# Performance work log

Measured on AMD Instinct MI355X. Metric: run time of the kernel, lower is better.

Reference implementation:

```python
import jax, jax.numpy as jnp
import numpy as np
import math

S, B, D = 2048, 2, 1024
H = 16
DH = D // H
WIN = 256
DIL = 1


def setup_inputs() -> dict:
    key = jax.random.key(0)
    ks = jax.random.split(key, 10)
    std = 1.0 / math.sqrt(D)
    return {
        "x": jax.random.normal(ks[0], (S, B, D), jnp.float32),
        "beta": jax.random.normal(ks[1], (H,), jnp.float32) * 0.02,
        "Wq": jax.random.normal(ks[2], (D, D), jnp.float32) * std,
        "bq": jnp.zeros((D,), jnp.float32),
        "Wk": jax.random.normal(ks[3], (D, D), jnp.float32) * std,
        "bk": jnp.zeros((D,), jnp.float32),
        "Wv": jax.random.normal(ks[4], (D, D), jnp.float32) * std,
        "bv": jnp.zeros((D,), jnp.float32),
        "Wo": jax.random.normal(ks[5], (D, D), jnp.float32) * std,
        "bo": jnp.zeros((D,), jnp.float32),
    }


def _split_heads(t):
    # (S, B, D) -> (B*H, S, DH), matching rearrange 's b (h d) -> (b h) s d'
    return t.reshape(S, B, H, DH).transpose(1, 2, 0, 3).reshape(B * H, S, DH)


def reference(x, beta, Wq, bq, Wk, bk, Wv, bv, Wo, bo):
    q = _split_heads(x @ Wq + bq)
    k = _split_heads(x @ Wk + bk)
    v = _split_heads(x @ Wv + bv)

    # per-head learnable temperature: q / (sqrt(d_head) * exp(beta))
    beta_exp = jnp.tile(jnp.exp(beta), B)  # (B*H,), head index = z % H
    q = q / (jnp.sqrt(jnp.asarray(DH, x.dtype)) * beta_exp)[:, None, None]

    # causal dilated windowed mask
    idx = jnp.arange(S)
    diff = idx[:, None] - idx[None, :]
    allowed = (diff >= 0) & (diff <= DIL * (WIN - 1)) & (diff % DIL == 0)
    mask = jnp.where(allowed, jnp.asarray(0.0, x.dtype), jnp.asarray(-jnp.inf, x.dtype))

    scores = jnp.einsum('zqd,zkd->zqk', q, k) + mask[None]
    # attention sink: extra zero-logit column absorbing probability mass
    scores = jnp.concatenate([scores, jnp.zeros((B * H, S, 1), scores.dtype)], axis=-1)
    attn = jax.nn.softmax(scores, axis=-1)[..., :-1]

    out = jnp.einsum('zqk,zkd->zqd', attn, v)
    # (B*H, S, DH) -> (S, B, D)
    out = out.reshape(B, H, S, DH).transpose(2, 0, 1, 3).reshape(S, B, D)
    return out @ Wo + bo
```

## Files before the change

kernel.cpp:

```cpp
#include <hip/hip_runtime.h>
#include <math.h>

#define S_LEN  2048
#define BATCH  2
#define DM     1024
#define NHEAD  16
#define DHEAD  64
#define WIN    256
#define MROWS  4096

#define KP   72
#define PPAD 68

typedef __attribute__((ext_vector_type(8))) short bf16x8;
typedef __attribute__((ext_vector_type(4))) float f32x4;

__device__ __forceinline__ unsigned short f2b(float f) {
    unsigned int u = __float_as_uint(f);
    return (unsigned short)((u + 0x7fffu + ((u >> 16) & 1u)) >> 16);
}
__device__ __forceinline__ void gld16(const void* g, void* l) {
    __builtin_amdgcn_global_load_lds(
        (const __attribute__((address_space(1))) void*)g,
        (__attribute__((address_space(3))) void*)l, 16, 0, 0);
}
__device__ __forceinline__ bf16x8 pack8(float4 a, float4 b) {
    bf16x8 r;
    r[0] = (short)f2b(a.x); r[1] = (short)f2b(a.y);
    r[2] = (short)f2b(a.z); r[3] = (short)f2b(a.w);
    r[4] = (short)f2b(b.x); r[5] = (short)f2b(b.y);
    r[6] = (short)f2b(b.z); r[7] = (short)f2b(b.w);
    return r;
}

__global__ __launch_bounds__(256)
void cvtx(const float* __restrict__ x, unsigned short* __restrict__ xb)
{
    const int i = (blockIdx.x * 256 + threadIdx.x) * 4;
    float4 f = *(const float4*)(x + i);
    ushort4 o; o.x = f2b(f.x); o.y = f2b(f.y); o.z = f2b(f.z); o.w = f2b(f.w);
    *(ushort4*)(xb + i) = o;
}

__global__ __launch_bounds__(256)
void twcvt4(const float* __restrict__ W0, const float* __restrict__ W1,
            const float* __restrict__ W2, const float* __restrict__ W3,
            unsigned short* __restrict__ T0, unsigned short* __restrict__ T1,
            unsigned short* __restrict__ T2, unsigned short* __restrict__ T3)
{
    const int zz = blockIdx.z;
    const float* W = (zz == 0) ? W0 : (zz == 1) ? W1 : (zz == 2) ? W2 : W3;
    unsigned short* WT = (zz == 0) ? T0 : (zz == 1) ? T1 : (zz == 2) ? T2 : T3;

    __shared__ float t32[32][33];
    const int bx = blockIdx.x * 32;
    const int by = blockIdx.y * 32;
    const int c  = threadIdx.x & 31;
    const int r0 = threadIdx.x >> 5;
#pragma unroll
    for (int p = 0; p < 4; ++p)
        t32[r0 + 8 * p][c] = W[(size_t)(by + r0 + 8 * p) * DM + bx + c];
    __syncthreads();
#pragma unroll
    for (int p = 0; p < 4; ++p)
        WT[(size_t)(bx + r0 + 8 * p) * DM + by + c] = f2b(t32[c][r0 + 8 * p]);
}

__global__ __launch_bounds__(256)
void gemm_mfma(const unsigned short* __restrict__ A,
               const unsigned short* __restrict__ BT,
               const float* __restrict__ bias,
               const float* __restrict__ bias2,
               const float* __restrict__ beta,
               float* __restrict__ Cf,
               unsigned short* __restrict__ Cb,
               int mode)
{
    __shared__ unsigned short As[128 * 32];
    __shared__ unsigned short Bs[128 * 32];

    const int t  = threadIdx.x;
    const int wv = t >> 6, ln = t & 63;
    const int rowBase = blockIdx.y * 128;
    const int colBase = blockIdx.x * 128;

    const int m16 = ln & 15, g = ln >> 4;
    const int wr = wv >> 1, wc = wv & 1;
    const int swz = m16 & 3;

    const int lr = ln >> 2;
    const int lq = (ln & 3) ^ (lr & 3);
    const unsigned short* ga = A  + (size_t)(rowBase + wv * 16 + lr) * DM + lq * 8;
    const unsigned short* gb = BT + (size_t)(colBase + wv * 16 + lr) * DM + lq * 8;
    unsigned short* la0 = As + wv * 512;
    unsigned short* la1 = la0 + 2048;
    unsigned short* lb0 = Bs + wv * 512;
    unsigned short* lb1 = lb0 + 2048;

    f32x4 acc[4][4];
#pragma unroll
    for (int u = 0; u < 4; ++u)
#pragma unroll
        for (int v = 0; v < 4; ++v)
            acc[u][v] = (f32x4){0.f, 0.f, 0.f, 0.f};

    for (int kb = 0; kb < DM; kb += 32) {
        gld16(ga + kb, la0);
        gld16(ga + (size_t)64 * DM + kb, la1);
        gld16(gb + kb, lb0);
        gld16(gb + (size_t)64 * DM + kb, lb1);
        __syncthreads();

        bf16x8 af[4], bfr[4];
#pragma unroll
        for (int u = 0; u < 4; ++u)
            af[u] = *(const bf16x8*)&As[(wr * 64 + u * 16 + m16) * 32 + ((g ^ swz) * 8)];
#pragma unroll
        for (int v = 0; v < 4; ++v)
            bfr[v] = *(const bf16x8*)&Bs[(wc * 64 + v * 16 + m16) * 32 + ((g ^ swz) * 8)];
#pragma unroll
        for (int u = 0; u < 4; ++u)
#pragma unroll
            for (int v = 0; v < 4; ++v)
                acc[u][v] = __builtin_amdgcn_mfma_f32_16x16x32_bf16(
                    af[u], bfr[v], acc[u][v], 0, 0, 0);
        __syncthreads();
    }

    const int q4 = g * 4;
    if (mode == 0) {
#pragma unroll
        for (int v = 0; v < 4; ++v) {
            const int col = colBase + wc * 64 + v * 16 + m16;
            const float bi = bias[col];
#pragma unroll
            for (int u = 0; u < 4; ++u)
#pragma unroll
                for (int r = 0; r < 4; ++r) {
                    const int row = rowBase + wr * 64 + u * 16 + q4 + r;
                    Cf[(size_t)row * DM + col] = acc[u][v][r] + bi;
                }
        }
    } else if (mode == 1) {
#pragma unroll
        for (int v = 0; v < 4; ++v) {
            const int col  = colBase + wc * 64 + v * 16 + m16;
            const bool isq = (col < DM);
            const int h    = (col >> 6) & (NHEAD - 1);
            const int dh   = col & 63;
            const float bi = isq ? bias[col] : bias2[col - DM];
            const float sc = isq ? 0.125f * __expf(-beta[h]) : 1.0f;
            unsigned short* base = Cb + (isq ? 0 : (size_t)MROWS * DM);
#pragma unroll
            for (int u = 0; u < 4; ++u)
#pragma unroll
                for (int r = 0; r < 4; ++r) {
                    const int row = rowBase + wr * 64 + u * 16 + q4 + r;
                    const int s = row >> 1, bb = row & 1;
                    const int z = bb * NHEAD + h;
                    base[((size_t)z * S_LEN + s) * DHEAD + dh] =
                        f2b((acc[u][v][r] + bi) * sc);
                }
        }
    } else {
#pragma unroll
        for (int u = 0; u < 4; ++u)
#pragma unroll
            for (int r = 0; r < 4; ++r) {
                const int row = rowBase + wr * 64 + u * 16 + q4 + r;
                const int hh = row >> 6, dh = row & 63;
                const float bi = bias[row];
#pragma unroll
                for (int v = 0; v < 4; ++v) {
                    const int col = colBase + wc * 64 + v * 16 + m16;
                    const int s = col >> 1, bb = col & 1;
                    Cb[((size_t)(bb * NHEAD + hh) * DHEAD + dh) * S_LEN + s] =
                        f2b(acc[u][v][r] + bi);
                }
            }
    }
}

__global__ __launch_bounds__(256, 4)
void attn_mfma(const unsigned short* __restrict__ q,
               const unsigned short* __restrict__ k,
               const unsigned short* __restrict__ vt,
               unsigned short* __restrict__ ao)
{
    __shared__ unsigned short Ks[64 * KP];
    __shared__ unsigned short Vs[64 * KP];
    __shared__ float Ps[64][PPAD];

    const int t   = threadIdx.x;
    const int wv  = t >> 6, ln = t & 63;
    const int m16 = ln & 15, g = ln >> 4;
    const int z   = blockIdx.y;
    const int q0  = blockIdx.x * 64;
    const size_t zbase = (size_t)z * S_LEN * DHEAD;

    const unsigned short* qrow = q + zbase + (size_t)(q0 + wv * 16 + m16) * DHEAD;
    bf16x8 qf0 = *(const bf16x8*)(qrow + g * 8);
    bf16x8 qf1 = *(const bf16x8*)(qrow + 32 + g * 8);

    f32x4 oacc[4];
#pragma unroll
    for (int v4 = 0; v4 < 4; ++v4) oacc[v4] = (f32x4){0.f, 0.f, 0.f, 0.f};
    float mr[4], lr[4];
#pragma unroll
    for (int r = 0; r < 4; ++r) { mr[r] = 0.f; lr[r] = 1.f; }

    for (int c = 0; c < 5; ++c) {
        const int kb = q0 - 256 + c * 64;
        if (kb < 0) continue;
        __syncthreads();

#pragma unroll
        for (int i = 0; i < 2; ++i) {
            const int id  = t + 256 * i;
            const int row = id >> 3;
            const int co  = (id & 7) * 8;
            *(bf16x8*)&Ks[row * KP + co] =
                *(const bf16x8*)(k + zbase + (size_t)(kb + row) * DHEAD + co);
            *(bf16x8*)&Vs[row * KP + co] =
                *(const bf16x8*)(vt + ((size_t)z * DHEAD + row) * S_LEN + kb + co);
        }
        __syncthreads();

        f32x4 sacc[4];
#pragma unroll
        for (int v4 = 0; v4 < 4; ++v4) {
            sacc[v4] = (f32x4){0.f, 0.f, 0.f, 0.f};
            bf16x8 kf0 = *(const bf16x8*)&Ks[(v4 * 16 + m16) * KP + g * 8];
            sacc[v4] = __builtin_amdgcn_mfma_f32_16x16x32_bf16(qf0, kf0, sacc[v4], 0, 0, 0);
            bf16x8 kf1 = *(const bf16x8*)&Ks[(v4 * 16 + m16) * KP + 32 + g * 8];
            sacc[v4] = __builtin_amdgcn_mfma_f32_16x16x32_bf16(qf1, kf1, sacc[v4], 0, 0, 0);
        }

        const bool mhi = (c == 4), mlo = (c == 0);
#pragma unroll
        for (int r = 0; r < 4; ++r) {
            const int ig = q0 + wv * 16 + g * 4 + r;
            float sv[4];
            float smax = -1e30f;
#pragma unroll
            for (int v4 = 0; v4 < 4; ++v4) {
                const int jg = kb + v4 * 16 + m16;
                float x = sacc[v4][r];
                const bool valid = (!mhi || jg <= ig) && (!mlo || jg >= ig - (WIN - 1));
                x = valid ? x : -1e30f;
                sv[v4] = x;
                smax = fmaxf(smax, x);
            }
#pragma unroll
            for (int off = 1; off < 16; off <<= 1)
                smax = fmaxf(smax, __shfl_xor(smax, off, 64));
            const float mnew  = fmaxf(mr[r], smax);
            const float alpha = __expf(mr[r] - mnew);
            float rsum = 0.f;
#pragma unroll
            for (int v4 = 0; v4 < 4; ++v4) {
                const float pp = __expf(sv[v4] - mnew);
                Ps[wv * 16 + g * 4 + r][v4 * 16 + m16] = pp;
                rsum += pp;
            }
#pragma unroll
            for (int off = 1; off < 16; off <<= 1)
                rsum += __shfl_xor(rsum, off, 64);
            lr[r] = lr[r] * alpha + rsum;
            mr[r] = mnew;
#pragma unroll
            for (int v4 = 0; v4 < 4; ++v4) oacc[v4][r] *= alpha;
        }
        __syncthreads();

        const float* prow = &Ps[wv * 16 + m16][0];
        bf16x8 pf0 = pack8(*(const float4*)(prow + g * 8),
                           *(const float4*)(prow + g * 8 + 4));
        bf16x8 pf1 = pack8(*(const float4*)(prow + 32 + g * 8),
                           *(const float4*)(prow + 32 + g * 8 + 4));
#pragma unroll
        for (int v4 = 0; v4 < 4; ++v4) {
            bf16x8 vf0 = *(const bf16x8*)&Vs[(v4 * 16 + m16) * KP + g * 8];
            oacc[v4] = __builtin_amdgcn_mfma_f32_16x16x32_bf16(pf0, vf0, oacc[v4], 0, 0, 0);
            bf16x8 vf1 = *(const bf16x8*)&Vs[(v4 * 16 + m16) * KP + 32 + g * 8];
            oacc[v4] = __builtin_amdgcn_mfma_f32_16x16x32_bf16(pf1, vf1, oacc[v4], 0, 0, 0);
        }
    }

    const int bb = z >> 4, h = z & 15;
#pragma unroll
    for (int r = 0; r < 4; ++r) {
        const int ig  = q0 + wv * 16 + g * 4 + r;
        const float inv = 1.f / lr[r];
#pragma unroll
        for (int v4 = 0; v4 < 4; ++v4)
            ao[(size_t)(ig * BATCH + bb) * DM + h * DHEAD + v4 * 16 + m16] =
                f2b(oacc[v4][r] * inv);
    }
}

extern "C" void kernel_launch(void* const* d_in, const int* in_sizes, int n_in,
                              void* d_out, int out_size, void* d_ws, size_t ws_size,
                              hipStream_t stream)
{
    const float* x    = (const float*)d_in[0];
    const float* beta = (const float*)d_in[1];
    const float* Wq   = (const float*)d_in[2];
    const float* bq   = (const float*)d_in[3];
    const float* Wk   = (const float*)d_in[4];
    const float* bk   = (const float*)d_in[5];
    const float* Wv   = (const float*)d_in[6];
    const float* bv   = (const float*)d_in[7];
    const float* Wo   = (const float*)d_in[8];
    const float* bo   = (const float*)d_in[9];
    float* out = (float*)d_out;

    unsigned short* w = (unsigned short*)d_ws;
    const size_t seg = (size_t)MROWS * DM;
    unsigned short* qb  = w;
    unsigned short* kbf = w + seg;
    unsigned short* vtb = w + 2 * seg;
    unsigned short* ab  = w + 3 * seg;
    unsigned short* xb  = w + 4 * seg;
    unsigned short* wtq = w + 5 * seg;
    unsigned short* wtk = wtq + (size_t)DM * DM;
    unsigned short* wtv = wtk + (size_t)DM * DM;
    unsigned short* wto = wtv + (size_t)DM * DM;

    cvtx<<<4096, 256, 0, stream>>>(x, xb);
    twcvt4<<<dim3(32, 32, 4), 256, 0, stream>>>(Wq, Wk, Wv, Wo, wtq, wtk, wtv, wto);

    gemm_mfma<<<dim3(2048 / 128, MROWS / 128), 256, 0, stream>>>(
        xb, wtq, bq, bk, beta, nullptr, qb, 1);
    gemm_mfma<<<dim3(MROWS / 128, DM / 128), 256, 0, stream>>>(
        wtv, xb, bv, nullptr, beta, nullptr, vtb, 3);

    attn_mfma<<<dim3(S_LEN / 64, BATCH * NHEAD), 256, 0, stream>>>(qb, kbf, vtb, ab);

    gemm_mfma<<<dim3(DM / 128, MROWS / 128), 256, 0, stream>>>(
        ab, wto, bo, nullptr, beta, out, nullptr, 0);
}
```

Baseline: 194.3 us.

## Fuse V projection into QKV GEMM and transpose V in a separate kernel

The V projection moves into the same GEMM launch as Q and K, widened to 3072 output columns, so all three write head-split bf16 rows. This replaces the separate V GEMM, whose transposed epilogue wrote scattered strided values. A small LDS-based vtrans kernel then transposes V into the (z, dh, s) layout attention expects, with coalesced 16-byte stores. It reuses the x bf16 buffer for V^T and adds one kernel launch plus an extra round trip of V through memory.

```diff
diff --git a/kernel.cpp b/kernel.cpp
--- a/kernel.cpp
+++ b/kernel.cpp
@@ -67,10 +67,38 @@
 }
 
 __global__ __launch_bounds__(256)
+void vtrans(const unsigned short* __restrict__ v, unsigned short* __restrict__ vt)
+{
+    __shared__ unsigned short T[64 * 72];
+    const int z  = blockIdx.y;
+    const int s0 = blockIdx.x * 64;
+    const int t  = threadIdx.x;
+#pragma unroll
+    for (int i = 0; i < 2; ++i) {
+        const int id = t + 256 * i;
+        const int r  = id >> 3;
+        const int c8 = (id & 7) * 8;
+        *(bf16x8*)&T[r * 72 + c8] =
+            *(const bf16x8*)(v + ((size_t)z * S_LEN + s0 + r) * DHEAD + c8);
+    }
+    __syncthreads();
+    const int dh = t & 63, sg = t >> 6;
+#pragma unroll
+    for (int i = 0; i < 2; ++i) {
+        const int sb = (sg + 4 * i) * 8;
+        bf16x8 o;
+#pragma unroll
+        for (int e = 0; e < 8; ++e) o[e] = T[(sb + e) * 72 + dh];
+        *(bf16x8*)(vt + ((size_t)z * DHEAD + dh) * S_LEN + s0 + sb) = o;
+    }
+}
+
+__global__ __launch_bounds__(256)
 void gemm_mfma(const unsigned short* __restrict__ A,
                const unsigned short* __restrict__ BT,
-               const float* __restrict__ bias,
-               const float* __restrict__ bias2,
+               const float* __restrict__ b0,
+               const float* __restrict__ b1,
+               const float* __restrict__ b2,
                const float* __restrict__ beta,
                float* __restrict__ Cf,
                unsigned short* __restrict__ Cb,
@@ -132,7 +160,7 @@
 #pragma unroll
         for (int v = 0; v < 4; ++v) {
             const int col = colBase + wc * 64 + v * 16 + m16;
-            const float bi = bias[col];
+            const float bi = b0[col];
 #pragma unroll
             for (int u = 0; u < 4; ++u)
 #pragma unroll
@@ -141,16 +169,16 @@
                     Cf[(size_t)row * DM + col] = acc[u][v][r] + bi;
                 }
         }
-    } else if (mode == 1) {
+    } else {
 #pragma unroll
         for (int v = 0; v < 4; ++v) {
-            const int col  = colBase + wc * 64 + v * 16 + m16;
-            const bool isq = (col < DM);
-            const int h    = (col >> 6) & (NHEAD - 1);
-            const int dh   = col & 63;
-            const float bi = isq ? bias[col] : bias2[col - DM];
-            const float sc = isq ? 0.125f * __expf(-beta[h]) : 1.0f;
-            unsigned short* base = Cb + (isq ? 0 : (size_t)MROWS * DM);
+            const int col = colBase + wc * 64 + v * 16 + m16;
+            const int sec = col >> 10;
+            const int h   = (col >> 6) & (NHEAD - 1);
+            const int dh  = col & 63;
+            const float bi = (sec == 0 ? b0 : sec == 1 ? b1 : b2)[col & (DM - 1)];
+            const float sc = (sec == 0) ? 0.125f * __expf(-beta[h]) : 1.0f;
+            unsigned short* base = Cb + (size_t)sec * MROWS * DM;
 #pragma unroll
             for (int u = 0; u < 4; ++u)
 #pragma unroll
@@ -162,22 +190,6 @@
                         f2b((acc[u][v][r] + bi) * sc);
                 }
         }
-    } else {
-#pragma unroll
-        for (int u = 0; u < 4; ++u)
-#pragma unroll
-            for (int r = 0; r < 4; ++r) {
-                const int row = rowBase + wr * 64 + u * 16 + q4 + r;
-                const int hh = row >> 6, dh = row & 63;
-                const float bi = bias[row];
-#pragma unroll
-                for (int v = 0; v < 4; ++v) {
-                    const int col = colBase + wc * 64 + v * 16 + m16;
-                    const int s = col >> 1, bb = col & 1;
-                    Cb[((size_t)(bb * NHEAD + hh) * DHEAD + dh) * S_LEN + s] =
-                        f2b(acc[u][v][r] + bi);
-                }
-            }
     }
 }
 
@@ -318,25 +330,26 @@
     unsigned short* w = (unsigned short*)d_ws;
     const size_t seg = (size_t)MROWS * DM;
     unsigned short* qb  = w;
-    unsigned short* kbf = w + seg;
-    unsigned short* vtb = w + 2 * seg;
+    unsigned short* kb  = w + seg;
+    unsigned short* vb  = w + 2 * seg;
     unsigned short* ab  = w + 3 * seg;
     unsigned short* xb  = w + 4 * seg;
     unsigned short* wtq = w + 5 * seg;
     unsigned short* wtk = wtq + (size_t)DM * DM;
     unsigned short* wtv = wtk + (size_t)DM * DM;
     unsigned short* wto = wtv + (size_t)DM * DM;
+    unsigned short* vtb = xb;
 
     cvtx<<<4096, 256, 0, stream>>>(x, xb);
     twcvt4<<<dim3(32, 32, 4), 256, 0, stream>>>(Wq, Wk, Wv, Wo, wtq, wtk, wtv, wto);
 
-    gemm_mfma<<<dim3(2048 / 128, MROWS / 128), 256, 0, stream>>>(
-        xb, wtq, bq, bk, beta, nullptr, qb, 1);
-    gemm_mfma<<<dim3(MROWS / 128, DM / 128), 256, 0, stream>>>(
-        wtv, xb, bv, nullptr, beta, nullptr, vtb, 3);
-
-    attn_mfma<<<dim3(S_LEN / 64, BATCH * NHEAD), 256, 0, stream>>>(qb, kbf, vtb, ab);
+    gemm_mfma<<<dim3(3072 / 128, MROWS / 128), 256, 0, stream>>>(
+        xb, wtq, bq, bk, bv, beta, nullptr, qb, 1);
+
+    vtrans<<<dim3(S_LEN / 64, BATCH * NHEAD), 256, 0, stream>>>(vb, vtb);
+
+    attn_mfma<<<dim3(S_LEN / 64, BATCH * NHEAD), 256, 0, stream>>>(qb, kb, vtb, ab);
 
     gemm_mfma<<<dim3(DM / 128, MROWS / 128), 256, 0, stream>>>(
-        ab, wto, bo, nullptr, beta, out, nullptr, 0);
-}
+        ab, wto, bo, nullptr, nullptr, beta, out, nullptr, 0);
+}
```

Result: slower. 198.2 us (+2.1%).
